# Kernel tuning notes

Measured on AMD Instinct MI355X. Metric: run time of the kernel, lower is better.

## Reference

```python
import jax, jax.numpy as jnp
import numpy as np

# ---- static config (mirrors init_kwargs) ----
B, E, L, CH = 2, 512, 128, 256      # batch, encoding_channels, latent_dim, channels
W = 512                              # window_size
STEP = W // 2                        # 256
NC = W // 2 + 1                      # 257 rfft coeffs
RS = 32768                           # resonance_samples
NF = RS // STEP                      # 128 frames
BASE_RES = 0.5
RES_FACTOR = (1.0 - BASE_RES) * 0.999


def setup_inputs() -> dict:
    key = jax.random.key(0)
    ks = jax.random.split(key, 8)
    return {
        "latents": jax.random.normal(ks[0], (B, E, L), jnp.float32),
        "phase0_u": jax.random.uniform(ks[1], (B, 1, E, NC), jnp.float32),
        "noise_u": jax.random.uniform(ks[2], (B, NF, E, NC), jnp.float32),
        "Win": jax.random.normal(ks[3], (3, L, CH), jnp.float32) / np.float32(np.sqrt(L)),
        "b_in": jnp.zeros((3, CH), jnp.float32),
        "Wh": jax.random.normal(ks[4], (3, 2, CH, CH), jnp.float32) / np.float32(np.sqrt(CH)),
        "b_h": jnp.zeros((3, 2, CH), jnp.float32),
        "Wout": jax.random.normal(ks[5], (3, CH, NC), jnp.float32) / np.float32(np.sqrt(CH)),
        "b_out": jnp.zeros((3, NC), jnp.float32),
    }


def _ln(x):
    # LayerNorm over last dim, no learned affine
    m = jnp.mean(x, -1, keepdims=True)
    v = jnp.var(x, -1, keepdims=True)
    return (x - m) * jax.lax.rsqrt(v + 1e-5)


def _stacks(latents, Win, b_in, Wh, b_h, Wout, b_out):
    # three LinearOutputStacks (to_initial / to_resonance / to_phase_dither)
    h = jnp.einsum('bel,slc->sbec', latents, Win) + b_in[:, None, None, :]
    for k in range(2):
        h = _ln(jax.nn.leaky_relu(h, 0.2))
        h = jnp.einsum('sbec,scd->sbed', h, Wh[:, k]) + b_h[:, k, None, None, :]
    h = _ln(jax.nn.leaky_relu(h, 0.2))
    return jnp.einsum('sbec,scn->sben', h, Wout) + b_out[:, None, None, :]


def reference(latents, phase0_u, noise_u, Win, b_in, Wh, b_h, Wout, b_out):
    out3 = _stacks(latents, Win, b_in, Wh, b_h, Wout, b_out)  # [3,B,E,NC]
    initial, res_pre, dith_pre = out3[0], out3[1], out3[2]
    res = BASE_RES + jax.nn.sigmoid(res_pre) * RES_FACTOR      # (0.5, ~1.0)
    dither = jax.nn.sigmoid(dith_pre)

    t = jnp.arange(NF, dtype=jnp.float32)[None, :, None, None]  # [1,NF,1,1]
    # sequential decay  mag_t = initial * res^t  (fused cumprod)
    mags = initial[:, None] * jnp.exp(t * jnp.log(res)[:, None])  # [B,NF,E,NC]

    gd = jnp.linspace(0.0, np.pi, NC).astype(jnp.float32)        # group delay
    phase0 = (phase0_u * 2.0 - 1.0) * np.float32(np.pi)
    noise = (noise_u * 2.0 - 1.0) * np.float32(np.pi)
    noise = noise.at[:, 0].set(0.0)  # first frame has no dither step
    # sequential phase accumulation as cumsum
    phases = phase0 + t * gd + jnp.cumsum(dither[:, None] * noise, axis=1)

    frames = jax.lax.complex(mags * jnp.cos(phases), mags * jnp.sin(phases))
    windowed = jnp.fft.irfft(frames, n=W, axis=-1, norm='ortho')  # [B,NF,E,W]
    windowed = jnp.transpose(windowed, (0, 2, 1, 3))              # [B,E,NF,W]

    # overlap-add with Hann window, hop = STEP = W//2
    win = (0.5 - 0.5 * jnp.cos(2.0 * np.pi * jnp.arange(W) / W)).astype(jnp.float32)
    xw = windowed * win
    a = xw[..., :STEP].reshape(B, E, NF * STEP)
    b = xw[..., STEP:].reshape(B, E, NF * STEP)
    out = jnp.zeros((B, E, (NF + 1) * STEP), jnp.float32)
    out = out.at[..., :NF * STEP].add(a)
    out = out.at[..., STEP:].add(b)
    return out[..., :RS]  # [B,E,RS]
```

## Files before the change

kernel.cpp:

```cpp
#include <hip/hip_runtime.h>
#include <hip/hip_bf16.h>

#define PI_F 3.14159265358979323846f

typedef short  bf16x8 __attribute__((ext_vector_type(8)));
typedef unsigned short u16x8 __attribute__((ext_vector_type(8)));
typedef float  f32x4  __attribute__((ext_vector_type(4)));

#define OUT3_OFF  0
#define TPACK_OFF 3158016

static __device__ __forceinline__ unsigned short f2bf(float x) {
    unsigned int u = __float_as_uint(x);
    unsigned int r = (u + 0x7fffu + ((u >> 16) & 1u)) >> 16;
    return (unsigned short)r;
}

static __device__ __forceinline__ unsigned int pk_bf16(float a, float b) {
    unsigned int r;
    asm("v_cvt_pk_bf16_f32 %0, %1, %2" : "=v"(r) : "v"(a), "v"(b));
    return r;
}

static __device__ __forceinline__ float sigm(float x) {
    return 1.f / (1.f + expf(-x));
}

static __device__ __forceinline__ float bf_lo(unsigned int u) {
    return __uint_as_float(u << 16);
}
static __device__ __forceinline__ float bf_hi(unsigned int u) {
    return __uint_as_float(u & 0xffff0000u);
}


__device__ __forceinline__ void ln4(float (*buf)[256], float* mrow, float* rrow)
{
    const int tid = threadIdx.x;
    const int lane = tid & 63, wv = tid >> 6;
    if (wv < 4) {
        float s = 0.f, s2 = 0.f;
        #pragma unroll
        for (int j = 0; j < 4; j++) {
            float v = buf[wv][lane + 64*j];
            s += v; s2 += v*v;
        }
        #pragma unroll
        for (int o = 32; o > 0; o >>= 1) {
            s  += __shfl_xor(s,  o, 64);
            s2 += __shfl_xor(s2, o, 64);
        }
        if (lane == 0) {
            float m   = s * (1.f/256.f);
            float var = s2 * (1.f/256.f) - m*m;
            mrow[wv] = m;
            rrow[wv] = rsqrtf(var + 1e-5f);
        }
    }
    __syncthreads();
    #pragma unroll
    for (int idx = tid; idx < 1024; idx += 512) {
        int r = idx >> 8, cc = idx & 255;
        buf[r][cc] = (buf[r][cc] - mrow[r]) * rrow[r];
    }
    __syncthreads();
}

template<int KDIM>
__device__ __forceinline__ void mmv2(const float (*in)[KDIM],
                                     const float* __restrict__ W,
                                     const float* __restrict__ bias,
                                     float (*outb)[256])
{
    const int tid = threadIdx.x;
    const int c  = tid & 255;
    const int r0 = (tid >> 8) * 2;
    float acc[2] = {0.f, 0.f};
    const float* Wp = W + c;
    for (int l16 = 0; l16 < KDIM; l16 += 16) {
        float wbuf[16];
        #pragma unroll
        for (int j = 0; j < 16; j++) wbuf[j] = Wp[(size_t)(l16 + j)*256];
        #pragma unroll
        for (int q = 0; q < 4; q++) {
            f32x4 iq[2];
            #pragma unroll
            for (int r = 0; r < 2; r++) iq[r] = *(const f32x4*)&in[r0 + r][l16 + q*4];
            #pragma unroll
            for (int jj = 0; jj < 4; jj++)
                #pragma unroll
                for (int r = 0; r < 2; r++)
                    acc[r] = fmaf(iq[r][jj], wbuf[q*4 + jj], acc[r]);
        }
    }
    const float bb = bias[c];
    #pragma unroll
    for (int r = 0; r < 2; r++) {
        float v = acc[r] + bb;
        outb[r0 + r][c] = (v >= 0.f) ? v : 0.2f*v;
    }
}

__global__ __launch_bounds__(512) void mlp_kernel(
    const float* __restrict__ latents,
    const float* __restrict__ Win,  const float* __restrict__ b_in,
    const float* __restrict__ Wh,   const float* __restrict__ b_h,
    const float* __restrict__ Wout, const float* __restrict__ b_out,
    float* __restrict__ out3)
{
    __shared__ float bufA[4][128];
    __shared__ float bufB[4][256];
    __shared__ float bufC[4][256];
    __shared__ float mrow[4], rrow[4];

    const int tid  = threadIdx.x;
    const int s    = blockIdx.y;
    const int row0 = blockIdx.x * 4;
    const int c    = tid & 255;
    const int r0   = (tid >> 8) * 2;

    {
        int r = tid >> 7, l = tid & 127;
        bufA[r][l] = latents[(size_t)(row0 + r)*128 + l];
    }
    __syncthreads();

    mmv2<128>(bufA, Win + (size_t)s*128*256, b_in + s*256, bufB);
    __syncthreads();
    ln4(bufB, mrow, rrow);

    mmv2<256>(bufB, Wh + ((size_t)s*2 + 0)*256*256, b_h + (s*2 + 0)*256, bufC);
    __syncthreads();
    ln4(bufC, mrow, rrow);

    mmv2<256>(bufC, Wh + ((size_t)s*2 + 1)*256*256, b_h + (s*2 + 1)*256, bufB);
    __syncthreads();
    ln4(bufB, mrow, rrow);

    {
        float acc[2] = {0.f, 0.f};
        const float* Wp = Wout + (size_t)s*256*257 + c;
        for (int l16 = 0; l16 < 256; l16 += 16) {
            float wbuf[16];
            #pragma unroll
            for (int j = 0; j < 16; j++) wbuf[j] = Wp[(size_t)(l16 + j)*257];
            #pragma unroll
            for (int q = 0; q < 4; q++) {
                f32x4 iq[2];
                #pragma unroll
                for (int r = 0; r < 2; r++) iq[r] = *(const f32x4*)&bufB[r0 + r][l16 + q*4];
                #pragma unroll
                for (int jj = 0; jj < 4; jj++)
                    #pragma unroll
                    for (int r = 0; r < 2; r++)
                        acc[r] = fmaf(iq[r][jj], wbuf[q*4 + jj], acc[r]);
            }
        }
        float bb = b_out[s*257 + c];
        #pragma unroll
        for (int r = 0; r < 2; r++)
            out3[((size_t)s*1024 + row0 + r0 + r)*257 + c] = acc[r] + bb;

        if (tid < 4) {
            const int r = tid;
            float a = 0.f;
            const float* Wp2 = Wout + (size_t)s*256*257 + 256;
            for (int l = 0; l < 256; ++l)
                a = fmaf(bufB[r][l], Wp2[(size_t)l*257], a);
            out3[((size_t)s*1024 + row0 + r)*257 + 256] = a + b_out[s*257 + 256];
        }
    }
}

__global__ __launch_bounds__(256) void tpack_init(unsigned short* __restrict__ tp)
{
    int g = blockIdx.x * 256 + threadIdx.x;
    int tile = g >> 6, l = g & 63;
    int ks = tile >> 3;
    int wv = tile & 7;
    int wg = wv >> 1, p = wv & 1;
    u16x8 v;
    #pragma unroll
    for (int j = 0; j < 8; ++j) {
        int k2 = ks*32 + ((l >> 4) << 3) + j;
        int kap = (k2 >> 1) + 1;
        int w  = wg*32 + 2*(l & 15) + p;
        int m  = (kap * w) & 511;
        float ang = (float)m * (PI_F / 256.f);
        float sn, cn; sincosf(ang, &sn, &cn);
        v[j] = f2bf((k2 & 1) ? sn : cn);
    }
    *(u16x8*)(tp + (size_t)g * 8) = v;
}

__global__ __launch_bounds__(512, 4) void synth_row(
    const float* __restrict__ out3,
    const float* __restrict__ phase0_u,
    const float* __restrict__ noise_u,
    const unsigned short* __restrict__ tpack,
    float* __restrict__ out)
{
    __shared__ __align__(16) unsigned int lds_u[16896];
    __shared__ float a0s[64];
    __shared__ float a256s[64];
    __shared__ float pbuf[8][260];
    __shared__ float xs128[64];
    __shared__ float xs384[64];

    unsigned int* abtP = lds_u;
    unsigned int* abtQ = lds_u + 64*132;
    float*        xbf  = (float*)lds_u;

    const int tid = threadIdx.x;
    const int row = blockIdx.x;
    const int b   = row >> 9;
    const int e   = row & 511;

    const float inv = 0.04419417382415922f;

    float pr = 0.f, dith_ = 0.f, gdd = 0.f;
    if (tid <= 256) {
        float dpre = out3[((size_t)2*1024 + row)*257 + tid];
        dith_ = sigm(dpre);
        float gd = (float)tid * (1.f/512.f);
        gdd = gd - 0.5f*dith_;
        pr  = phase0_u[(size_t)row*257 + tid] - 0.5f;
    }
    float m2 = 0.f, res2_ = 0.f;
    if (tid == 256) {
        float i2 = out3[((size_t)0*1024 + row)*257 + 256];
        float r2 = out3[((size_t)1*1024 + row)*257 + 256];
        res2_ = 0.5f + 0.4995f * sigm(r2);
        m2    = inv * i2;
    }

    const int kc = tid & 255;
    const int j0 = (tid >> 8) * 4;
    float m_base, rp1, rp2, rp3, res8;
    float bsgn = -1.f;
    unsigned int* tgt = abtP;
    {
        float ini  = out3[((size_t)0*1024 + row)*257 + kc];
        float rpre = out3[((size_t)1*1024 + row)*257 + kc];
        float res  = 0.5f + 0.4995f * sigm(rpre);
        float cs   = (kc == 0 ? 1.f : 2.f) * inv;
        rp1 = res;
        rp2 = res * res;
        rp3 = rp2 * res;
        float res4 = rp2 * rp2;
        res8 = res4 * res4;
        m_base = cs * ini;
        if (j0 == 4) m_base *= res4;
        if (kc >= 129)     { tgt = abtQ + (255 - kc); bsgn = 1.f; }
        else if (kc >= 1)  { tgt = abtP + (kc - 1); }
    }

    const float* nrow = noise_u + ((size_t)b*128*512 + e)*257;
    const size_t nstride = (size_t)512*257;

    float h1 = 0.f, h2 = 0.f;
    {
        float c0 = __builtin_amdgcn_cosf((float)tid * (1.f/512.f));
        h1 = 0.5f - 0.5f*c0;
        h2 = 0.5f + 0.5f*c0;
    }
    const float sgn = (tid & 1) ? -1.f : 1.f;
    float tail = 0.f;

    const int l  = tid & 63;
    const int wv = tid >> 6;
    const int m0 = l & 15;
    const int ac = l >> 4;
    const int wsrc = (wv >> 1)*32 + 2*m0 + (wv & 1);
    const int c1 = wsrc;
    const int c2 = wsrc + 256;
    const int c3 = 256 - wsrc;
    const int c4 = 512 - wsrc;
    const bool c4ok = (wsrc != 0);
    const int4* abtP4 = (const int4*)abtP;
    const int4* abtQ4 = (const int4*)abtQ;
    const int4* abtR4 = (wv & 1) ? abtQ4 : abtP4;
    const int4* Tp    = (const int4*)tpack;
    const unsigned int S   = 0x80008000u;
    const unsigned int B31 = 0x80000000u;

    for (int sweep = 0; sweep < 2; ++sweep) {
        const int F0 = sweep * 64;

        for (int g = 0; g < 8; ++g) {
            if (tid <= 256) {
                float nzb[8];
                #pragma unroll
                for (int j = 0; j < 8; ++j) {
                    int t = F0 + g*8 + j;
                    nzb[j] = (t >= 1) ? __builtin_nontemporal_load(
                                            &nrow[(size_t)t*nstride + tid]) : 0.5f;
                }
                #pragma unroll
                for (int j = 0; j < 8; ++j) {
                    int t = F0 + g*8 + j;
                    if (t >= 1) pr += fmaf(dith_, nzb[j], gdd);
                    pbuf[j][tid] = pr;
                    if (tid == 256) {
                        if (t >= 1) m2 *= res2_;
                        float fr = pr - floorf(pr);
                        a256s[g*8 + j] = m2 * __builtin_amdgcn_cosf(fr);
                    }
                }
            } else if (g == 0 && tid >= 448) {
                abtQ[(tid - 448)*132 + 127] = 0;
            }
            __syncthreads();

            {
                const int fb = g*8 + j0;
                float mv[4];
                mv[0] = m_base;
                mv[1] = m_base * rp1;
                mv[2] = m_base * rp2;
                mv[3] = m_base * rp3;
                #pragma unroll
                for (int q = 0; q < 4; ++q) {
                    float p  = pbuf[j0 + q][kc];
                    float fr = p - floorf(p);
                    float sn = __builtin_amdgcn_sinf(fr);
                    float cn = __builtin_amdgcn_cosf(fr);
                    float a  = mv[q] * cn;
                    if (kc == 0) {
                        a0s[fb + q] = a;
                    } else {
                        float bv = bsgn * mv[q] * sn;
                        tgt[(fb + q)*132] = pk_bf16(a, bv);
                    }
                }
                m_base *= res8;
            }
            __syncthreads();
        }

        {
            #pragma unroll
            for (int i = 0; i < 16; ++i) {
                int idx = tid + i*512;
                int f  = idx >> 7, ki = idx & 127;
                int o  = f*132 + ki;
                unsigned int up = abtP[o];
                unsigned int uq = abtQ[o];
                float aP = bf_lo(up), bP = bf_hi(up);
                float aQ = bf_lo(uq), bQ = bf_hi(uq);
                abtP[o] = pk_bf16(aP + aQ, bP + bQ);
                abtQ[o] = pk_bf16(aP - aQ, bP - bQ);
            }
        }
        __syncthreads();

        f32x4 acc1[4], acc2[4], acc3[4], acc4[4];
        #pragma unroll
        for (int mt = 0; mt < 4; ++mt) {
            acc1[mt] = (f32x4){0.f, 0.f, 0.f, 0.f};
            acc2[mt] = (f32x4){0.f, 0.f, 0.f, 0.f};
            acc3[mt] = (f32x4){0.f, 0.f, 0.f, 0.f};
            acc4[mt] = (f32x4){0.f, 0.f, 0.f, 0.f};
        }
        {
            const int r0g = m0*33 + ac;
            for (int ks = 0; ks < 8; ++ks) {
                int4 bi = Tp[(size_t)((ks*8 + wv) << 6) + l];
                bf16x8 B = *(bf16x8*)&bi;
                #pragma unroll
                for (int mt = 0; mt < 4; ++mt) {
                    int4 t = abtR4[r0g + mt*528 + ks*4];
                    acc1[mt] = __builtin_amdgcn_mfma_f32_16x16x32_bf16(*(bf16x8*)&t, B, acc1[mt], 0, 0, 0);
                    t.x ^= S;   t.z ^= S;
                    acc2[mt] = __builtin_amdgcn_mfma_f32_16x16x32_bf16(*(bf16x8*)&t, B, acc2[mt], 0, 0, 0);
                    t.x ^= B31; t.y ^= B31; t.z ^= B31; t.w ^= B31;
                    acc3[mt] = __builtin_amdgcn_mfma_f32_16x16x32_bf16(*(bf16x8*)&t, B, acc3[mt], 0, 0, 0);
                    t.x ^= S;   t.z ^= S;
                    acc4[mt] = __builtin_amdgcn_mfma_f32_16x16x32_bf16(*(bf16x8*)&t, B, acc4[mt], 0, 0, 0);
                }
            }
        }

        {
            const int f8 = tid >> 3;
            const int i8 = tid & 7;
            float s128 = 0.f, s384 = 0.f;
            #pragma unroll
            for (int q = 0; q < 16; ++q) {
                int ki = i8*16 + q;
                unsigned int ue = abtP[f8*132 + ki];
                if ((q + 1) & 1) {
                    float sg = ((q + 1) & 2) ? -1.f : 1.f;
                    float bsum = bf_hi(ue);
                    s128 += sg * bsum;
                    s384 -= sg * bsum;
                } else {
                    float sg = ((q + 1) & 2) ? -1.f : 1.f;
                    float asum = bf_lo(ue);
                    s128 += sg * asum;
                    s384 += sg * asum;
                }
            }
            #pragma unroll
            for (int o = 1; o < 8; o <<= 1) {
                s128 += __shfl_xor(s128, o, 64);
                s384 += __shfl_xor(s384, o, 64);
            }
            if (i8 == 0) { xs128[f8] = s128; xs384[f8] = s384; }
        }
        __syncthreads();

        #pragma unroll
        for (int h = 0; h < 2; ++h) {
            #pragma unroll
            for (int mt2 = 0; mt2 < 2; ++mt2) {
                int mtg = 2*h + mt2;
                #pragma unroll
                for (int r = 0; r < 4; ++r) {
                    int f_loc = mt2*16 + ac*4 + r;
                    float* xr = &xbf[f_loc*516];
                    xr[c1] = acc1[mtg][r];
                    xr[c2] = acc2[mtg][r];
                    xr[c3] = acc3[mtg][r];
                    if (c4ok) xr[c4] = acc4[mtg][r];
                }
            }
            if (tid < 32) {
                xbf[tid*516 + 128] = xs128[h*32 + tid];
                xbf[tid*516 + 384] = xs384[h*32 + tid];
            }
            __syncthreads();
            if (tid < 256) {
                float* orow = out + (size_t)row*32768 + (size_t)(F0 + h*32)*256 + tid;
                #pragma unroll
                for (int f = 0; f < 32; ++f) {
                    int hf = h*32 + f;
                    float s  = a0s[hf] + sgn * a256s[hf];
                    float x1 = xbf[f*516 + tid] + s;
                    float x2 = xbf[f*516 + tid + 256] + s;
                    float v  = fmaf(x1, h1, tail);
                    tail = x2 * h2;
                    __builtin_nontemporal_store(v, &orow[f*256]);
                }
            }
            __syncthreads();
        }
    }
}


extern "C" void kernel_launch(void* const* d_in, const int* in_sizes, int n_in,
                              void* d_out, int out_size, void* d_ws, size_t ws_size,
                              hipStream_t stream)
{
    const float* latents  = (const float*)d_in[0];
    const float* phase0_u = (const float*)d_in[1];
    const float* noise_u  = (const float*)d_in[2];
    const float* Win      = (const float*)d_in[3];
    const float* b_in     = (const float*)d_in[4];
    const float* Wh       = (const float*)d_in[5];
    const float* b_h      = (const float*)d_in[6];
    const float* Wout     = (const float*)d_in[7];
    const float* b_out    = (const float*)d_in[8];

    unsigned char* ws = (unsigned char*)d_ws;
    float*          out3  = (float*)(ws + OUT3_OFF);
    unsigned short* tpack = (unsigned short*)(ws + TPACK_OFF);
    float*          out   = (float*)d_out;

    dim3 gA(256, 3);
    mlp_kernel<<<gA, 512, 0, stream>>>(latents, Win, b_in, Wh, b_h, Wout, b_out, out3);
    tpack_init<<<16, 256, 0, stream>>>(tpack);
    synth_row<<<1024, 512, 0, stream>>>(out3, phase0_u, noise_u, tpack, out);
}
```

Before: 168.8 us.

## Run MLP stacks on bf16 MFMA with split hi/lo precision and packed weights

Replaces the scalar FMA MLP kernel with a matrix-core version. Each weight and activation is split into bf16 high and low parts, and three MFMAs per product approximate fp32 accuracy. A new pre-pass kernel packs the weights into an MFMA-friendly tiled layout in workspace. Each block now processes 64 rows instead of 4, which improves weight reuse but leaves only 48 blocks in the grid, and it adds an extra kernel launch.

Result: no change. 166.0 us (-1.7%).

```diff
diff --git a/kernel.cpp b/kernel.cpp
--- a/kernel.cpp
+++ b/kernel.cpp
@@ -9,6 +9,7 @@
 
 #define OUT3_OFF  0
 #define TPACK_OFF 3158016
+#define WPACK_OFF (3158016 + 65536)
 
 static __device__ __forceinline__ unsigned short f2bf(float x) {
     unsigned int u = __float_as_uint(x);
@@ -33,141 +34,189 @@
     return __uint_as_float(u & 0xffff0000u);
 }
 
-
-__device__ __forceinline__ void ln4(float (*buf)[256], float* mrow, float* rrow)
+__global__ __launch_bounds__(256) void wpack(
+    const float* __restrict__ Win, const float* __restrict__ Wh,
+    const float* __restrict__ Wout, unsigned short* __restrict__ wp)
 {
-    const int tid = threadIdx.x;
-    const int lane = tid & 63, wv = tid >> 6;
-    if (wv < 4) {
-        float s = 0.f, s2 = 0.f;
-        #pragma unroll
-        for (int j = 0; j < 4; j++) {
-            float v = buf[wv][lane + 64*j];
-            s += v; s2 += v*v;
-        }
-        #pragma unroll
-        for (int o = 32; o > 0; o >>= 1) {
-            s  += __shfl_xor(s,  o, 64);
-            s2 += __shfl_xor(s2, o, 64);
-        }
-        if (lane == 0) {
-            float m   = s * (1.f/256.f);
-            float var = s2 * (1.f/256.f) - m*m;
-            mrow[wv] = m;
-            rrow[wv] = rsqrtf(var + 1e-5f);
-        }
-    }
-    __syncthreads();
+    int g = blockIdx.x * 256 + threadIdx.x;
+    int t = g >> 6, l = g & 63;
+    int s = t / 448, lt = t % 448;
+    int layer, base;
+    if (lt < 64)       { layer = 0; base = 0;   }
+    else if (lt < 192) { layer = 1; base = 64;  }
+    else if (lt < 320) { layer = 2; base = 192; }
+    else               { layer = 3; base = 320; }
+    int local = lt - base, ks = local >> 4, nt = local & 15;
+
+    u16x8 hv, lv;
     #pragma unroll
-    for (int idx = tid; idx < 1024; idx += 512) {
-        int r = idx >> 8, cc = idx & 255;
-        buf[r][cc] = (buf[r][cc] - mrow[r]) * rrow[r];
-    }
-    __syncthreads();
-}
-
-template<int KDIM>
-__device__ __forceinline__ void mmv2(const float (*in)[KDIM],
-                                     const float* __restrict__ W,
-                                     const float* __restrict__ bias,
-                                     float (*outb)[256])
-{
-    const int tid = threadIdx.x;
-    const int c  = tid & 255;
-    const int r0 = (tid >> 8) * 2;
-    float acc[2] = {0.f, 0.f};
-    const float* Wp = W + c;
-    for (int l16 = 0; l16 < KDIM; l16 += 16) {
-        float wbuf[16];
-        #pragma unroll
-        for (int j = 0; j < 16; j++) wbuf[j] = Wp[(size_t)(l16 + j)*256];
-        #pragma unroll
-        for (int q = 0; q < 4; q++) {
-            f32x4 iq[2];
-            #pragma unroll
-            for (int r = 0; r < 2; r++) iq[r] = *(const f32x4*)&in[r0 + r][l16 + q*4];
-            #pragma unroll
-            for (int jj = 0; jj < 4; jj++)
-                #pragma unroll
-                for (int r = 0; r < 2; r++)
-                    acc[r] = fmaf(iq[r][jj], wbuf[q*4 + jj], acc[r]);
-        }
-    }
-    const float bb = bias[c];
-    #pragma unroll
-    for (int r = 0; r < 2; r++) {
-        float v = acc[r] + bb;
-        outb[r0 + r][c] = (v >= 0.f) ? v : 0.2f*v;
-    }
-}
-
-__global__ __launch_bounds__(512) void mlp_kernel(
+    for (int j = 0; j < 8; ++j) {
+        int k = ks*32 + ((l >> 4) << 3) + j;
+        int n = nt*16 + (l & 15);
+        float w;
+        if (layer == 0)      w = Win[(size_t)s*32768 + k*256 + n];
+        else if (layer == 1) w = Wh[((size_t)s*2 + 0)*65536 + k*256 + n];
+        else if (layer == 2) w = Wh[((size_t)s*2 + 1)*65536 + k*256 + n];
+        else                 w = Wout[(size_t)s*65792 + k*257 + n];
+        unsigned int ph = pk_bf16(w, 0.f);
+        float fh = bf_lo(ph);
+        hv[j] = (unsigned short)(ph & 0xffffu);
+        lv[j] = (unsigned short)(pk_bf16(w - fh, 0.f) & 0xffffu);
+    }
+    *(u16x8*)(wp + (size_t)(t*2    )*512 + l*8) = hv;
+    *(u16x8*)(wp + (size_t)(t*2 + 1)*512 + l*8) = lv;
+}
+
+__global__ __launch_bounds__(512) void mlp_mfma(
     const float* __restrict__ latents,
-    const float* __restrict__ Win,  const float* __restrict__ b_in,
-    const float* __restrict__ Wh,   const float* __restrict__ b_h,
-    const float* __restrict__ Wout, const float* __restrict__ b_out,
+    const float* __restrict__ b_in, const float* __restrict__ b_h,
+    const float* __restrict__ b_out, const float* __restrict__ Wout,
+    const unsigned short* __restrict__ wp,
     float* __restrict__ out3)
 {
-    __shared__ float bufA[4][128];
-    __shared__ float bufB[4][256];
-    __shared__ float bufC[4][256];
-    __shared__ float mrow[4], rrow[4];
+    __shared__ float xs[64*260];
+    __shared__ unsigned int xh[64*132];
+    __shared__ unsigned int xl[64*132];
+    __shared__ float mrow[64], rrow[64];
 
     const int tid  = threadIdx.x;
     const int s    = blockIdx.y;
-    const int row0 = blockIdx.x * 4;
-    const int c    = tid & 255;
-    const int r0   = (tid >> 8) * 2;
-
-    {
-        int r = tid >> 7, l = tid & 127;
-        bufA[r][l] = latents[(size_t)(row0 + r)*128 + l];
+    const int row0 = blockIdx.x * 64;
+    const int l  = tid & 63;
+    const int wv = tid >> 6;
+    const int m0 = l & 15;
+    const int ac = l >> 4;
+
+    const int4* Wp4 = (const int4*)wp;
+    const int4* xh4 = (const int4*)xh;
+    const int4* xl4 = (const int4*)xl;
+
+    #pragma unroll
+    for (int i = 0; i < 8; ++i) {
+        int idx = tid + i*512;
+        int r = idx >> 6, kp = idx & 63;
+        const float* lp = latents + (size_t)(row0 + r)*128 + 2*kp;
+        float x0 = lp[0], x1 = lp[1];
+        unsigned int u = pk_bf16(x0, x1);
+        xh[r*132 + kp] = u;
+        xl[r*132 + kp] = pk_bf16(x0 - bf_lo(u), x1 - bf_hi(u));
     }
     __syncthreads();
 
-    mmv2<128>(bufA, Win + (size_t)s*128*256, b_in + s*256, bufB);
-    __syncthreads();
-    ln4(bufB, mrow, rrow);
-
-    mmv2<256>(bufB, Wh + ((size_t)s*2 + 0)*256*256, b_h + (s*2 + 0)*256, bufC);
-    __syncthreads();
-    ln4(bufC, mrow, rrow);
-
-    mmv2<256>(bufC, Wh + ((size_t)s*2 + 1)*256*256, b_h + (s*2 + 1)*256, bufB);
-    __syncthreads();
-    ln4(bufB, mrow, rrow);
-
-    {
-        float acc[2] = {0.f, 0.f};
-        const float* Wp = Wout + (size_t)s*256*257 + c;
-        for (int l16 = 0; l16 < 256; l16 += 16) {
-            float wbuf[16];
-            #pragma unroll
-            for (int j = 0; j < 16; j++) wbuf[j] = Wp[(size_t)(l16 + j)*257];
-            #pragma unroll
-            for (int q = 0; q < 4; q++) {
-                f32x4 iq[2];
-                #pragma unroll
-                for (int r = 0; r < 2; r++) iq[r] = *(const f32x4*)&bufB[r0 + r][l16 + q*4];
-                #pragma unroll
-                for (int jj = 0; jj < 4; jj++)
-                    #pragma unroll
-                    for (int r = 0; r < 2; r++)
-                        acc[r] = fmaf(iq[r][jj], wbuf[q*4 + jj], acc[r]);
-            }
-        }
-        float bb = b_out[s*257 + c];
+    for (int L = 0; L < 4; ++L) {
+        const int kt    = (L == 0) ? 4 : 8;
+        const int tbase = s*448 + ((L == 0) ? 0 : (L == 1) ? 64 : (L == 2) ? 192 : 320);
+
+        f32x4 acc[4][2];
         #pragma unroll
-        for (int r = 0; r < 2; r++)
-            out3[((size_t)s*1024 + row0 + r0 + r)*257 + c] = acc[r] + bb;
-
-        if (tid < 4) {
-            const int r = tid;
-            float a = 0.f;
-            const float* Wp2 = Wout + (size_t)s*256*257 + 256;
-            for (int l = 0; l < 256; ++l)
-                a = fmaf(bufB[r][l], Wp2[(size_t)l*257], a);
-            out3[((size_t)s*1024 + row0 + r)*257 + 256] = a + b_out[s*257 + 256];
+        for (int mt = 0; mt < 4; ++mt) {
+            acc[mt][0] = (f32x4){0.f, 0.f, 0.f, 0.f};
+            acc[mt][1] = (f32x4){0.f, 0.f, 0.f, 0.f};
+        }
+
+        for (int ks = 0; ks < kt; ++ks) {
+            const int t0 = tbase + ks*16 + wv*2;
+            int4 bh0 = Wp4[(size_t)(t0*2    )*64 + l];
+            int4 bl0 = Wp4[(size_t)(t0*2 + 1)*64 + l];
+            int4 bh1 = Wp4[(size_t)(t0*2 + 2)*64 + l];
+            int4 bl1 = Wp4[(size_t)(t0*2 + 3)*64 + l];
+            bf16x8 BH0 = *(bf16x8*)&bh0, BL0 = *(bf16x8*)&bl0;
+            bf16x8 BH1 = *(bf16x8*)&bh1, BL1 = *(bf16x8*)&bl1;
+            #pragma unroll
+            for (int mt = 0; mt < 4; ++mt) {
+                int4 ah = xh4[(m0 + 16*mt)*33 + ks*4 + ac];
+                int4 al = xl4[(m0 + 16*mt)*33 + ks*4 + ac];
+                bf16x8 AH = *(bf16x8*)&ah, AL = *(bf16x8*)&al;
+                acc[mt][0] = __builtin_amdgcn_mfma_f32_16x16x32_bf16(AH, BH0, acc[mt][0], 0, 0, 0);
+                acc[mt][0] = __builtin_amdgcn_mfma_f32_16x16x32_bf16(AH, BL0, acc[mt][0], 0, 0, 0);
+                acc[mt][0] = __builtin_amdgcn_mfma_f32_16x16x32_bf16(AL, BH0, acc[mt][0], 0, 0, 0);
+                acc[mt][1] = __builtin_amdgcn_mfma_f32_16x16x32_bf16(AH, BH1, acc[mt][1], 0, 0, 0);
+                acc[mt][1] = __builtin_amdgcn_mfma_f32_16x16x32_bf16(AH, BL1, acc[mt][1], 0, 0, 0);
+                acc[mt][1] = __builtin_amdgcn_mfma_f32_16x16x32_bf16(AL, BH1, acc[mt][1], 0, 0, 0);
+            }
+        }
+
+        if (L < 3) {
+            const float* bias = (L == 0) ? (b_in + s*256) : (b_h + (s*2 + (L-1))*256);
+            const float bb0 = bias[wv*32 + m0];
+            const float bb1 = bias[wv*32 + 16 + m0];
+            #pragma unroll
+            for (int mt = 0; mt < 4; ++mt)
+                #pragma unroll
+                for (int r = 0; r < 4; ++r) {
+                    int row = mt*16 + ac*4 + r;
+                    float v0 = acc[mt][0][r] + bb0;
+                    float v1 = acc[mt][1][r] + bb1;
+                    v0 = (v0 >= 0.f) ? v0 : 0.2f*v0;
+                    v1 = (v1 >= 0.f) ? v1 : 0.2f*v1;
+                    xs[row*260 + wv*32 + m0]      = v0;
+                    xs[row*260 + wv*32 + 16 + m0] = v1;
+                }
+            __syncthreads();
+
+            #pragma unroll
+            for (int i = 0; i < 8; ++i) {
+                int row = wv*8 + i;
+                float s1 = 0.f, s2 = 0.f;
+                #pragma unroll
+                for (int j = 0; j < 4; ++j) {
+                    float v = xs[row*260 + l + 64*j];
+                    s1 += v; s2 += v*v;
+                }
+                #pragma unroll
+                for (int o = 32; o > 0; o >>= 1) {
+                    s1 += __shfl_xor(s1, o, 64);
+                    s2 += __shfl_xor(s2, o, 64);
+                }
+                if (l == 0) {
+                    float m   = s1 * (1.f/256.f);
+                    float var = s2 * (1.f/256.f) - m*m;
+                    mrow[row] = m;
+                    rrow[row] = rsqrtf(var + 1e-5f);
+                }
+            }
+            __syncthreads();
+
+            #pragma unroll
+            for (int i = 0; i < 16; ++i) {
+                int idx = tid + i*512;
+                int r = idx >> 7, kp = idx & 127;
+                float mm = mrow[r], rr = rrow[r];
+                float u = (xs[r*260 + 2*kp    ] - mm) * rr;
+                float v = (xs[r*260 + 2*kp + 1] - mm) * rr;
+                unsigned int uh = pk_bf16(u, v);
+                xh[r*132 + kp] = uh;
+                xl[r*132 + kp] = pk_bf16(u - bf_lo(uh), v - bf_hi(uh));
+            }
+            __syncthreads();
+        } else {
+            const float* bo = b_out + s*257;
+            #pragma unroll
+            for (int mt = 0; mt < 4; ++mt)
+                #pragma unroll
+                for (int r = 0; r < 4; ++r) {
+                    int row = mt*16 + ac*4 + r;
+                    float* op = out3 + ((size_t)s*1024 + row0 + row)*257;
+                    op[wv*32 + m0]      = acc[mt][0][r] + bo[wv*32 + m0];
+                    op[wv*32 + 16 + m0] = acc[mt][1][r] + bo[wv*32 + 16 + m0];
+                }
+            {
+                int r  = tid >> 3;
+                int c8 = tid & 7;
+                float mm = mrow[r], rr = rrow[r];
+                float p = 0.f;
+                const float* w2 = Wout + (size_t)s*65792 + 256;
+                #pragma unroll
+                for (int j = 0; j < 32; ++j) {
+                    int cc = c8*32 + j;
+                    p = fmaf((xs[r*260 + cc] - mm) * rr, w2[(size_t)cc*257], p);
+                }
+                p += __shfl_xor(p, 1, 64);
+                p += __shfl_xor(p, 2, 64);
+                p += __shfl_xor(p, 4, 64);
+                if (c8 == 0)
+                    out3[((size_t)s*1024 + row0 + r)*257 + 256] = p + b_out[s*257 + 256];
+            }
         }
     }
 }
@@ -466,10 +515,12 @@
     unsigned char* ws = (unsigned char*)d_ws;
     float*          out3  = (float*)(ws + OUT3_OFF);
     unsigned short* tpack = (unsigned short*)(ws + TPACK_OFF);
+    unsigned short* wp    = (unsigned short*)(ws + WPACK_OFF);
     float*          out   = (float*)d_out;
 
-    dim3 gA(256, 3);
-    mlp_kernel<<<gA, 512, 0, stream>>>(latents, Win, b_in, Wh, b_h, Wout, b_out, out3);
+    wpack<<<336, 256, 0, stream>>>(Win, Wh, Wout, wp);
+    dim3 gM(16, 3);
+    mlp_mfma<<<gM, 512, 0, stream>>>(latents, b_in, b_h, b_out, Wout, wp, out3);
     tpack_init<<<16, 256, 0, stream>>>(tpack);
     synth_row<<<1024, 512, 0, stream>>>(out3, phase0_u, noise_u, tpack, out);
 }
```
